# Kernel optimization log

Hardware: AMD Instinct MI355X
Metric: run time of the kernel (lower is better)

The kernel has to match this reference:

```python
import jax, jax.numpy as jnp
import numpy as np

HIDDEN = 2048
NH = 32        # query heads
NKV = 4        # kv heads
D = 128        # head dim
T = 2048       # tokens
WINDOW = 512   # sliding window
EPS = 1e-6
THETA = 1000000.0
SCALE = D ** -0.5


def setup_inputs() -> dict:
    key = jax.random.key(0)
    k1, k2, k3 = jax.random.split(key, 3)
    return {
        "positions": jnp.arange(T, dtype=jnp.int64) if jax.config.jax_enable_x64 else jnp.arange(T, dtype=jnp.int32),
        "hidden_states": jax.random.normal(k1, (T, HIDDEN), dtype=jnp.float32),
        "w_qkv": jax.random.normal(k2, (HIDDEN, (NH + 2 * NKV) * D), dtype=jnp.float32) * 0.02,
        "w_o": jax.random.normal(k3, (NH * D, HIDDEN), dtype=jnp.float32) * 0.02,
        "q_norm_w": jnp.ones((D,), dtype=jnp.float32),
        "k_norm_w": jnp.ones((D,), dtype=jnp.float32),
    }


def _rms_norm(x, w):
    # x: [..., D]; per-head RMSNorm
    var = jnp.mean(x * x, axis=-1, keepdims=True)
    return x * jax.lax.rsqrt(var + EPS) * w


def _rope(x, positions):
    # x: [T, H, D], neox-style rotary over full head dim
    inv_freq = 1.0 / (THETA ** (jnp.arange(0, D, 2, dtype=jnp.float32) / D))  # [D/2]
    freqs = positions.astype(jnp.float32)[:, None] * inv_freq                 # [T, D/2]
    cos = jnp.cos(freqs)[:, None, :]
    sin = jnp.sin(freqs)[:, None, :]
    x1, x2 = x[..., : D // 2], x[..., D // 2 :]
    return jnp.concatenate([x1 * cos - x2 * sin, x2 * cos + x1 * sin], axis=-1)


def reference(positions, hidden_states, w_qkv, w_o, q_norm_w, k_norm_w):
    qkv = hidden_states @ w_qkv                                   # [T, (NH+2NKV)*D]
    q, k, v = jnp.split(qkv, [NH * D, (NH + NKV) * D], axis=-1)
    q = _rms_norm(q.reshape(T, NH, D), q_norm_w)
    k = _rms_norm(k.reshape(T, NKV, D), k_norm_w)
    v = v.reshape(T, NKV, D)
    q = _rope(q, positions)
    k = _rope(k, positions)
    # GQA: expand kv heads to query heads
    rep = NH // NKV
    k = jnp.repeat(k, rep, axis=1)                                # [T, NH, D]
    v = jnp.repeat(v, rep, axis=1)
    scores = jnp.einsum("qhd,khd->hqk", q, k) * SCALE             # [NH, T, T]
    i = jnp.arange(T)[:, None]
    j = jnp.arange(T)[None, :]
    mask = (j <= i) & (i - j < WINDOW)                            # causal sliding window
    scores = jnp.where(mask[None, :, :], scores, jnp.finfo(scores.dtype).min)
    probs = jax.nn.softmax(scores, axis=-1)
    out = jnp.einsum("hqk,khd->qhd", probs, v).reshape(T, NH * D)
    return out @ w_o
```

## Files before the change

### kernel.cpp

```cpp
#include <hip/hip_runtime.h>
#include <math.h>

#define T      2048
#define HIDDEN 2048
#define NH     32
#define NKV    4
#define D      128
#define WINDOW 512
#define QKVW   ((NH + 2 * NKV) * D)
#define ODIM   (NH * D)
#define EPS    1e-6f
#define SCALE  0.08838834764831845f
#define PSTR   68
#define ESTR   136
#define QMUL   ((float)(0.08838834764831845 * 1.4426950408889634))
#define MLOG2E 5.7707801635558536f

typedef _Float16 f16x8 __attribute__((ext_vector_type(8)));
typedef float    f32x4 __attribute__((ext_vector_type(4)));


__global__ __launch_bounds__(256)
void pack_a(const float* __restrict__ A, _Float16* __restrict__ out,
            int M, int K) {
  const int cid = blockIdx.x * 256 + threadIdx.x;
  const int c = cid & 63;
  const int tile = cid >> 6;
  const int mtg = tile % (M >> 4);
  const int kt = tile / (M >> 4);
  const int m = c & 15, q = c >> 4;
  const float* src = A + (size_t)(mtg * 16 + m) * K + kt * 32 + q * 8;
  const float4 a = *(const float4*)src;
  const float4 b = *(const float4*)(src + 4);
  f16x8 h;
  h[0] = (_Float16)a.x; h[1] = (_Float16)a.y; h[2] = (_Float16)a.z; h[3] = (_Float16)a.w;
  h[4] = (_Float16)b.x; h[5] = (_Float16)b.y; h[6] = (_Float16)b.z; h[7] = (_Float16)b.w;
  *(f16x8*)(out + (size_t)cid * 8) = h;
}

__global__ __launch_bounds__(256)
void pack_b(const float* __restrict__ B, _Float16* __restrict__ out,
            int K, int N) {
  const int cid = blockIdx.x * 256 + threadIdx.x;
  const int c = cid & 63;
  const int tile = cid >> 6;
  const int ntg = tile % (N >> 4);
  const int kt = tile / (N >> 4);
  const int n = c & 15, q = c >> 4;
  const float* src = B + (size_t)(kt * 32 + q * 8) * N + ntg * 16 + n;
  f16x8 h;
#pragma unroll
  for (int j = 0; j < 8; ++j) h[j] = (_Float16)src[(size_t)j * N];
  *(f16x8*)(out + (size_t)cid * 8) = h;
}

__device__ __forceinline__ void gl2lds16(const void* g, void* l) {
  __builtin_amdgcn_global_load_lds((const __attribute__((address_space(1))) void*)g,
                                   (__attribute__((address_space(3))) void*)l,
                                   16, 0, 0);
}

__global__ __launch_bounds__(256)
void gemm_qkv(const _Float16* __restrict__ Apk, const _Float16* __restrict__ Bpk,
              const float* __restrict__ qnw, const float* __restrict__ knw,
              const float* __restrict__ cosT, const float* __restrict__ sinT,
              _Float16* __restrict__ Qpk, _Float16* __restrict__ Kpk,
              _Float16* __restrict__ Vpk) {
  constexpr int AT = 8, BT = 8, RT = 4, CT = 4;
  constexpr int NKT = HIDDEN / 32;
  __shared__ _Float16 SM[17920];
  _Float16* As = SM;
  _Float16* Bs = SM + 8192;

  const int tid = threadIdx.x;
  const int lane = tid & 63;
  const int wv = tid >> 6;
  const int wr = wv & 1, wc = wv >> 1;
  const int l15 = lane & 15;
  const int l4 = lane >> 4;
  const int bx = blockIdx.x, by = blockIdx.y;

  f32x4 acc[RT][CT];
#pragma unroll
  for (int i = 0; i < RT; ++i)
#pragma unroll
    for (int j = 0; j < CT; ++j) acc[i][j] = (f32x4)0.f;

  const size_t Astep = (size_t)(T >> 4) * 1024;
  const size_t Bstep = (size_t)(QKVW >> 4) * 1024;
  const char* Ag = (const char*)Apk + (size_t)(by * AT) * 1024 + lane * 16;
  const char* Bg = (const char*)Bpk + (size_t)(bx * BT) * 1024 + lane * 16;

  for (int kt2 = 0; kt2 < NKT; kt2 += 2) {
    const char* a0 = Ag + (size_t)kt2 * Astep;
    const char* b0 = Bg + (size_t)kt2 * Bstep;
#pragma unroll
    for (int t = wv; t < 2 * (AT + BT); t += 4) {
      const int half = t >= (AT + BT);
      const int tt = half ? t - (AT + BT) : t;
      if (tt < AT)
        gl2lds16(a0 + half * Astep + (size_t)tt * 1024,
                 (char*)As + (half * AT + tt) * 1024);
      else
        gl2lds16(b0 + half * Bstep + (size_t)(tt - AT) * 1024,
                 (char*)Bs + (half * BT + (tt - AT)) * 1024);
    }
    __syncthreads();
#pragma unroll
    for (int h2 = 0; h2 < 2; ++h2) {
      f16x8 af[RT], bf[CT];
#pragma unroll
      for (int i = 0; i < RT; ++i)
        af[i] = *(const f16x8*)((const char*)As + (h2 * AT + wr * RT + i) * 1024 + lane * 16);
#pragma unroll
      for (int j = 0; j < CT; ++j)
        bf[j] = *(const f16x8*)((const char*)Bs + (h2 * BT + wc * CT + j) * 1024 + lane * 16);
#pragma unroll
      for (int i = 0; i < RT; ++i)
#pragma unroll
        for (int j = 0; j < CT; ++j)
          acc[i][j] = __builtin_amdgcn_mfma_f32_16x16x32_f16(af[i], bf[j], acc[i][j], 0, 0, 0);
    }
    __syncthreads();
  }

  _Float16* ex = SM;
  float* sums = (float*)(SM + 17408);

  if (bx < NH + NKV) {
    const bool isq = bx < NH;
    const float* w = isq ? qnw : knw;
    const float omul = isq ? QMUL : 1.0f;

#pragma unroll
    for (int i = 0; i < RT; ++i)
#pragma unroll
      for (int r = 0; r < 4; ++r) {
        float s = acc[i][0][r] * acc[i][0][r] + acc[i][1][r] * acc[i][1][r]
                + acc[i][2][r] * acc[i][2][r] + acc[i][3][r] * acc[i][3][r];
        s += __shfl_xor(s, 1); s += __shfl_xor(s, 2);
        s += __shfl_xor(s, 4); s += __shfl_xor(s, 8);
        if (l15 == 0) sums[wc * 128 + wr * 64 + i * 16 + l4 * 4 + r] = s;
      }
    __syncthreads();

    float wcol[4];
#pragma unroll
    for (int j = 0; j < 4; ++j) wcol[j] = w[wc * 64 + j * 16 + l15];
#pragma unroll
    for (int i = 0; i < RT; ++i)
#pragma unroll
      for (int r = 0; r < 4; ++r) {
        const int row = wr * 64 + i * 16 + l4 * 4 + r;
        const float rn = 1.0f / sqrtf((sums[row] + sums[128 + row]) * (1.0f / D) + EPS);
#pragma unroll
        for (int j = 0; j < 4; ++j) {
          acc[i][j][r] *= rn * wcol[j];
          ex[row * ESTR + wc * 64 + j * 16 + l15] = (_Float16)acc[i][j][r];
        }
      }
    __syncthreads();

    const float sgn = (wc == 0) ? -1.f : 1.f;
    const int poff = wc ? 0 : 64;
#pragma unroll
    for (int i = 0; i < RT; ++i)
#pragma unroll
      for (int r = 0; r < 4; ++r) {
        const int row = wr * 64 + i * 16 + l4 * 4 + r;
        const int t = by * 128 + row;
#pragma unroll
        for (int j = 0; j < 4; ++j) {
          const int jc = j * 16 + l15;
          const float c = cosT[t * 64 + jc];
          const float s = sinT[t * 64 + jc];
          const float pr = (float)ex[row * ESTR + jc + poff];
          acc[i][j][r] = acc[i][j][r] * c + sgn * pr * s;
        }
      }
    __syncthreads();

#pragma unroll
    for (int i = 0; i < RT; ++i)
#pragma unroll
      for (int r = 0; r < 4; ++r) {
        const int row = wr * 64 + i * 16 + l4 * 4 + r;
#pragma unroll
        for (int j = 0; j < 4; ++j)
          ex[row * ESTR + wc * 64 + j * 16 + l15] = (_Float16)(acc[i][j][r] * omul);
      }
    __syncthreads();

    const int hl = isq ? bx : bx - NH;
    _Float16* dst0 = isq ? Qpk : Kpk;
#pragma unroll
    for (int u = 0; u < 2; ++u) {
      const int qtl = wv * 2 + u;
#pragma unroll
      for (int ds = 0; ds < 4; ++ds) {
        const f16x8 frag = *(const f16x8*)(ex + (qtl * 16 + l15) * ESTR + ds * 32 + l4 * 8);
        *(f16x8*)(dst0 + ((size_t)(hl * 128 + by * 8 + qtl) * 4 + ds) * 512 + lane * 8) = frag;
      }
    }
  } else {
    const int kvh = bx - NH - NKV;
#pragma unroll
    for (int i = 0; i < RT; ++i)
#pragma unroll
      for (int r = 0; r < 4; ++r) {
        const int row = wr * 64 + i * 16 + l4 * 4 + r;
#pragma unroll
        for (int j = 0; j < 4; ++j)
          ex[row * ESTR + wc * 64 + j * 16 + l15] = (_Float16)acc[i][j][r];
      }
    __syncthreads();
#pragma unroll
    for (int u = 0; u < 8; ++u) {
      const int idx = wv + 4 * u;
      const int dt = idx & 7, ks = (idx >> 3) & 1, ktl = idx >> 4;
      f16x8 h8;
#pragma unroll
      for (int jj = 0; jj < 8; ++jj)
        h8[jj] = ex[(ktl * 64 + ks * 32 + l4 * 8 + jj) * ESTR + dt * 16 + l15];
      *(f16x8*)(Vpk + (((size_t)(kvh * 32 + by * 2 + ktl) * 2 + ks) * 8 + dt) * 512 + lane * 8) = h8;
    }
  }
}

template<int BN>
__global__ __launch_bounds__(256)
void gemm_f16(const _Float16* __restrict__ Apk, const _Float16* __restrict__ Bpk,
              float* __restrict__ C0, float* __restrict__ C1,
              int M, int N, int nkt) {
  constexpr int BM = 128;
  constexpr int AT = BM / 16;
  constexpr int BT = BN / 16;
  constexpr int RT = 4;
  constexpr int CT = BN / 32;
  __shared__ _Float16 As[2 * AT * 512];
  __shared__ _Float16 Bs[2 * BT * 512];

  const int tid = threadIdx.x;
  const int lane = tid & 63;
  const int wv = tid >> 6;
  const int wr = wv & 1, wc = wv >> 1;
  const int kt0 = blockIdx.z * nkt;
  float* __restrict__ C = blockIdx.z ? C1 : C0;

  f32x4 acc[RT][CT];
#pragma unroll
  for (int i = 0; i < RT; ++i)
#pragma unroll
    for (int j = 0; j < CT; ++j) acc[i][j] = (f32x4)0.f;

  const size_t Astep = (size_t)(M >> 4) * 1024;
  const size_t Bstep = (size_t)(N >> 4) * 1024;
  const char* Ag = (const char*)Apk + (size_t)kt0 * Astep +
                   (size_t)(blockIdx.y * AT) * 1024 + lane * 16;
  const char* Bg = (const char*)Bpk + (size_t)kt0 * Bstep +
                   (size_t)(blockIdx.x * BT) * 1024 + lane * 16;

  for (int kt2 = 0; kt2 < nkt; kt2 += 2) {
    const char* a0 = Ag + (size_t)kt2 * Astep;
    const char* b0 = Bg + (size_t)kt2 * Bstep;
#pragma unroll
    for (int t = wv; t < 2 * (AT + BT); t += 4) {
      const int half = t >= (AT + BT);
      const int tt = half ? t - (AT + BT) : t;
      if (tt < AT)
        gl2lds16(a0 + half * Astep + (size_t)tt * 1024,
                 (char*)As + (half * AT + tt) * 1024);
      else
        gl2lds16(b0 + half * Bstep + (size_t)(tt - AT) * 1024,
                 (char*)Bs + (half * BT + (tt - AT)) * 1024);
    }
    __syncthreads();

#pragma unroll
    for (int h2 = 0; h2 < 2; ++h2) {
      f16x8 af[RT], bf[CT];
#pragma unroll
      for (int i = 0; i < RT; ++i)
        af[i] = *(const f16x8*)((const char*)As + (h2 * AT + wr * RT + i) * 1024 + lane * 16);
#pragma unroll
      for (int j = 0; j < CT; ++j)
        bf[j] = *(const f16x8*)((const char*)Bs + (h2 * BT + wc * CT + j) * 1024 + lane * 16);
#pragma unroll
      for (int i = 0; i < RT; ++i)
#pragma unroll
        for (int j = 0; j < CT; ++j)
          acc[i][j] = __builtin_amdgcn_mfma_f32_16x16x32_f16(af[i], bf[j], acc[i][j], 0, 0, 0);
    }
    __syncthreads();
  }

  const int row0 = blockIdx.y * BM + wr * 64 + ((lane >> 4) << 2);
  const int col0 = blockIdx.x * BN + wc * (CT * 16) + (lane & 15);
#pragma unroll
  for (int i = 0; i < RT; ++i)
#pragma unroll
    for (int j = 0; j < CT; ++j) {
#pragma unroll
      for (int r = 0; r < 4; ++r)
        C[(size_t)(row0 + i * 16 + r) * N + col0 + j * 16] = acc[i][j][r];
    }
}

__global__ __launch_bounds__(256)
void reduce_add(const float4* __restrict__ a, const float4* __restrict__ b,
                float4* __restrict__ o, int n4) {
  for (int i = blockIdx.x * 256 + threadIdx.x; i < n4; i += gridDim.x * 256) {
    const float4 x = a[i], y = b[i];
    o[i] = make_float4(x.x + y.x, x.y + y.y, x.z + y.z, x.w + y.w);
  }
}

__global__ __launch_bounds__(64)
void rope_tables(const int* __restrict__ positions,
                 float* __restrict__ cosT, float* __restrict__ sinT) {
  const int j = threadIdx.x;
  const int p0 = blockIdx.x * 64;
  const float invf = (float)pow(1.0e6, -(double)j / 64.0);
#pragma unroll 4
  for (int i = 0; i < 64; ++i) {
    const int t = p0 + i;
    const float ang = (float)positions[t] * invf;
    cosT[t * 64 + j] = cosf(ang);
    sinT[t * 64 + j] = sinf(ang);
  }
}

__global__ __launch_bounds__(256)
void attn_mfma(const _Float16* __restrict__ Qpk, const _Float16* __restrict__ Kpk,
               const _Float16* __restrict__ Vpk, _Float16* __restrict__ Ap2) {
  const int h = blockIdx.x;
  const int q0 = blockIdx.y * 128;
  const int kvh = h >> 3;
  const int tid = threadIdx.x;
  const int lane = tid & 63;
  const int wv = tid >> 6;
  const int l15 = lane & 15;
  const int l4 = lane >> 4;

  __shared__ _Float16 SM[8192 + 8192 + 4 * 32 * PSTR];
  _Float16* Ks = SM;
  _Float16* Vs = SM + 8192;
  _Float16* Pw = SM + 16384 + wv * 32 * PSTR;

  f16x8 qfA[4], qfB[4];
  {
    const _Float16* qa = Qpk + ((size_t)h * 128 + (q0 >> 4) + wv * 2) * 2048 + lane * 8;
#pragma unroll
    for (int ds = 0; ds < 4; ++ds) {
      qfA[ds] = *(const f16x8*)(qa + ds * 512);
      qfB[ds] = *(const f16x8*)(qa + 2048 + ds * 512);
    }
  }

  f16x8 ones;
#pragma unroll
  for (int j = 0; j < 8; ++j) ones[j] = (_Float16)1.0f;

  f32x4 OA[8], OB[8];
#pragma unroll
  for (int dt = 0; dt < 8; ++dt) { OA[dt] = (f32x4)0.f; OB[dt] = (f32x4)0.f; }
  f32x4 LA = (f32x4)0.f, LB = (f32x4)0.f;

  int kstart = q0 - (WINDOW - 1);
  if (kstart < 0) kstart = 0;
  kstart &= ~63;

  for (int kt = kstart; kt < q0 + 128; kt += 64) {
    __syncthreads();
    const _Float16* Kg = Kpk + ((size_t)kvh * 128 + (kt >> 4)) * 2048 + lane * 8;
    const _Float16* Vg = Vpk + ((size_t)kvh * 32 + (kt >> 6)) * 8192 + lane * 8;
#pragma unroll
    for (int t = wv; t < 16; t += 4) {
      gl2lds16(Kg + t * 512, (char*)Ks + t * 1024);
      gl2lds16(Vg + t * 512, (char*)Vs + t * 1024);
    }
    __syncthreads();

    f32x4 sA[4], sB[4];
#pragma unroll
    for (int nt = 0; nt < 4; ++nt) { sA[nt] = (f32x4)(-MLOG2E); sB[nt] = (f32x4)(-MLOG2E); }
#pragma unroll
    for (int ds = 0; ds < 4; ++ds) {
#pragma unroll
      for (int nt = 0; nt < 4; ++nt) {
        const f16x8 kf = *(const f16x8*)(Ks + (nt * 4 + ds) * 512 + lane * 8);
        sA[nt] = __builtin_amdgcn_mfma_f32_16x16x32_f16(qfA[ds], kf, sA[nt], 0, 0, 0);
        sB[nt] = __builtin_amdgcn_mfma_f32_16x16x32_f16(qfB[ds], kf, sB[nt], 0, 0, 0);
      }
    }

    const int qbA = q0 + wv * 32 + l4 * 4;
    const int kb = kt + l15;
#pragma unroll
    for (int nt = 0; nt < 4; ++nt) {
      const int kidx = kb + nt * 16;
#pragma unroll
      for (int r = 0; r < 4; ++r) {
        float pA = __builtin_amdgcn_exp2f(sA[nt][r]);
        float pB = __builtin_amdgcn_exp2f(sB[nt][r]);
        pA = ((unsigned)(qbA + r - kidx) < WINDOW) ? pA : 0.f;
        pB = ((unsigned)(qbA + 16 + r - kidx) < WINDOW) ? pB : 0.f;
        Pw[(l4 * 4 + r) * PSTR + nt * 16 + l15] = (_Float16)pA;
        Pw[(16 + l4 * 4 + r) * PSTR + nt * 16 + l15] = (_Float16)pB;
      }
    }

#pragma unroll
    for (int ks = 0; ks < 2; ++ks) {
      const f16x8 pfA = *(const f16x8*)(Pw + l15 * PSTR + ks * 32 + l4 * 8);
      const f16x8 pfB = *(const f16x8*)(Pw + (16 + l15) * PSTR + ks * 32 + l4 * 8);
      LA = __builtin_amdgcn_mfma_f32_16x16x32_f16(pfA, ones, LA, 0, 0, 0);
      LB = __builtin_amdgcn_mfma_f32_16x16x32_f16(pfB, ones, LB, 0, 0, 0);
#pragma unroll
      for (int dt = 0; dt < 8; ++dt) {
        const f16x8 vf = *(const f16x8*)(Vs + (ks * 8 + dt) * 512 + lane * 8);
        OA[dt] = __builtin_amdgcn_mfma_f32_16x16x32_f16(pfA, vf, OA[dt], 0, 0, 0);
        OB[dt] = __builtin_amdgcn_mfma_f32_16x16x32_f16(pfB, vf, OB[dt], 0, 0, 0);
      }
    }
  }

  __syncthreads();
  _Float16* Tw = SM + wv * 16 * ESTR;
#pragma unroll
  for (int half = 0; half < 2; ++half) {
    const f32x4* O = half ? OB : OA;
    const f32x4  L = half ? LB : LA;
    float inv[4];
#pragma unroll
    for (int r = 0; r < 4; ++r) inv[r] = 1.0f / L[r];
#pragma unroll
    for (int dt = 0; dt < 8; ++dt)
#pragma unroll
      for (int r = 0; r < 4; ++r)
        Tw[(l4 * 4 + r) * ESTR + dt * 16 + l15] = (_Float16)(O[dt][r] * inv[r]);
    const int qt = (q0 >> 4) + wv * 2 + half;
#pragma unroll
    for (int ds = 0; ds < 4; ++ds) {
      const f16x8 frag = *(const f16x8*)(Tw + l15 * ESTR + ds * 32 + l4 * 8);
      *(f16x8*)(Ap2 + ((size_t)(h * 4 + ds) * 128 + qt) * 512 + lane * 8) = frag;
    }
  }
}

extern "C" void kernel_launch(void* const* d_in, const int* in_sizes, int n_in,
                              void* d_out, int out_size, void* d_ws, size_t ws_size,
                              hipStream_t stream) {
  const int*   positions = (const int*)d_in[0];
  const float* hidden    = (const float*)d_in[1];
  const float* w_qkv     = (const float*)d_in[2];
  const float* w_o       = (const float*)d_in[3];
  const float* q_norm_w  = (const float*)d_in[4];
  const float* k_norm_w  = (const float*)d_in[5];
  float* out = (float*)d_out;

  char* ws = (char*)d_ws;
  _Float16* Kpk = (_Float16*)ws;
  _Float16* Vpk = Kpk + (size_t)T * NKV * D;
  ws += (size_t)T * QKVW * 4;
  _Float16* Ap2 = (_Float16*)ws;
  float* P0 = (float*)(ws + (size_t)T * ODIM * 2);
  ws += (size_t)T * ODIM * 4;
  float* cosT = (float*)ws;  ws += (size_t)T * 64 * 4;
  float* sinT = (float*)ws;  ws += (size_t)T * 64 * 4;
  _Float16* Bp1 = (_Float16*)ws; ws += (size_t)HIDDEN * QKVW * 2;
  _Float16* Bp2 = (_Float16*)ws; ws += (size_t)ODIM * HIDDEN * 2;
  _Float16* Ah1 = (_Float16*)ws; ws += (size_t)T * HIDDEN * 2;
  _Float16* Qpk = (_Float16*)ws;
  float* P1 = (float*)Qpk;
  ws += (size_t)T * ODIM * 2;

  pack_a<<<dim3((size_t)T * HIDDEN / 8 / 256), 256, 0, stream>>>(hidden, Ah1, T, HIDDEN);
  pack_b<<<dim3((size_t)HIDDEN * QKVW / 8 / 256), 256, 0, stream>>>(w_qkv, Bp1, HIDDEN, QKVW);
  pack_b<<<dim3((size_t)ODIM * HIDDEN / 8 / 256), 256, 0, stream>>>(w_o, Bp2, ODIM, HIDDEN);
  rope_tables<<<dim3(T / 64), 64, 0, stream>>>(positions, cosT, sinT);

  gemm_qkv<<<dim3(QKVW / 128, T / 128), 256, 0, stream>>>(
      Ah1, Bp1, q_norm_w, k_norm_w, cosT, sinT, Qpk, Kpk, Vpk);

  attn_mfma<<<dim3(NH, T / 128), 256, 0, stream>>>(Qpk, Kpk, Vpk, Ap2);

  gemm_f16<128><<<dim3(HIDDEN / 128, T / 128, 2), 256, 0, stream>>>(
      Ap2, Bp2, P0, P1, T, HIDDEN, ODIM / 32 / 2);
  reduce_add<<<dim3(512), 256, 0, stream>>>((const float4*)P0, (const float4*)P1,
                                            (float4*)out, T * HIDDEN / 4);
}
```

Before: 323.6 us.

## Fuse pack/rope prep kernels and restructure QKV GEMM epilogue per-wave

Merges the three packing kernels and the rope-table kernel into one launch that dispatches work by block range. This removes launch overhead and lets the small rope work overlap with the packing. The QKV GEMM changes its wave layout so each wave owns 32 full rows (2x8 tiles) instead of a 2x2 split. RMSNorm and RoPE can then run in registers with a shuffle reduction and no block-wide syncs, and the V transpose uses per-wave LDS. In exchange, every wave now reads all B fragments per k-step, which raises LDS read traffic.

```diff
diff --git a/kernel.cpp b/kernel.cpp
--- a/kernel.cpp
+++ b/kernel.cpp
@@ -13,51 +13,79 @@
 #define SCALE  0.08838834764831845f
 #define PSTR   68
 #define ESTR   136
+#define VSTR   36
 #define QMUL   ((float)(0.08838834764831845 * 1.4426950408889634))
 #define MLOG2E 5.7707801635558536f
 
 typedef _Float16 f16x8 __attribute__((ext_vector_type(8)));
+typedef _Float16 f16x4 __attribute__((ext_vector_type(4)));
 typedef float    f32x4 __attribute__((ext_vector_type(4)));
 
-
-__global__ __launch_bounds__(256)
-void pack_a(const float* __restrict__ A, _Float16* __restrict__ out,
-            int M, int K) {
-  const int cid = blockIdx.x * 256 + threadIdx.x;
-  const int c = cid & 63;
-  const int tile = cid >> 6;
-  const int mtg = tile % (M >> 4);
-  const int kt = tile / (M >> 4);
-  const int m = c & 15, q = c >> 4;
-  const float* src = A + (size_t)(mtg * 16 + m) * K + kt * 32 + q * 8;
-  const float4 a = *(const float4*)src;
-  const float4 b = *(const float4*)(src + 4);
-  f16x8 h;
-  h[0] = (_Float16)a.x; h[1] = (_Float16)a.y; h[2] = (_Float16)a.z; h[3] = (_Float16)a.w;
-  h[4] = (_Float16)b.x; h[5] = (_Float16)b.y; h[6] = (_Float16)b.z; h[7] = (_Float16)b.w;
-  *(f16x8*)(out + (size_t)cid * 8) = h;
-}
-
-__global__ __launch_bounds__(256)
-void pack_b(const float* __restrict__ B, _Float16* __restrict__ out,
-            int K, int N) {
-  const int cid = blockIdx.x * 256 + threadIdx.x;
-  const int c = cid & 63;
-  const int tile = cid >> 6;
-  const int ntg = tile % (N >> 4);
-  const int kt = tile / (N >> 4);
-  const int n = c & 15, q = c >> 4;
-  const float* src = B + (size_t)(kt * 32 + q * 8) * N + ntg * 16 + n;
-  f16x8 h;
-#pragma unroll
-  for (int j = 0; j < 8; ++j) h[j] = (_Float16)src[(size_t)j * N];
-  *(f16x8*)(out + (size_t)cid * 8) = h;
-}
 
 __device__ __forceinline__ void gl2lds16(const void* g, void* l) {
   __builtin_amdgcn_global_load_lds((const __attribute__((address_space(1))) void*)g,
                                    (__attribute__((address_space(3))) void*)l,
                                    16, 0, 0);
+}
+
+#define NB_A  2048
+#define NB_B1 5120
+#define NB_B2 4096
+__global__ __launch_bounds__(256)
+void prep(const float* __restrict__ hidden, const float* __restrict__ w_qkv,
+          const float* __restrict__ w_o, const int* __restrict__ positions,
+          _Float16* __restrict__ Ah1, _Float16* __restrict__ Bp1,
+          _Float16* __restrict__ Bp2, float* __restrict__ cosT,
+          float* __restrict__ sinT) {
+  const int bx = blockIdx.x;
+  const int tid = threadIdx.x;
+  if (bx < NB_A) {
+    const int cid = bx * 256 + tid;
+    const int c = cid & 63;
+    const int tile = cid >> 6;
+    const int mtg = tile & (T / 16 - 1);
+    const int kt = tile >> 7;
+    const float* src = hidden + (size_t)(mtg * 16 + (c & 15)) * HIDDEN + kt * 32 + (c >> 4) * 8;
+    const float4 a = *(const float4*)src;
+    const float4 b = *(const float4*)(src + 4);
+    f16x8 h;
+    h[0] = (_Float16)a.x; h[1] = (_Float16)a.y; h[2] = (_Float16)a.z; h[3] = (_Float16)a.w;
+    h[4] = (_Float16)b.x; h[5] = (_Float16)b.y; h[6] = (_Float16)b.z; h[7] = (_Float16)b.w;
+    *(f16x8*)(Ah1 + (size_t)cid * 8) = h;
+  } else if (bx < NB_A + NB_B1) {
+    const int cid = (bx - NB_A) * 256 + tid;
+    const int c = cid & 63;
+    const int tile = cid >> 6;
+    const int ntg = tile % (QKVW >> 4);
+    const int kt = tile / (QKVW >> 4);
+    const float* src = w_qkv + (size_t)(kt * 32 + (c >> 4) * 8) * QKVW + ntg * 16 + (c & 15);
+    f16x8 h;
+#pragma unroll
+    for (int j = 0; j < 8; ++j) h[j] = (_Float16)src[(size_t)j * QKVW];
+    *(f16x8*)(Bp1 + (size_t)cid * 8) = h;
+  } else if (bx < NB_A + NB_B1 + NB_B2) {
+    const int cid = (bx - NB_A - NB_B1) * 256 + tid;
+    const int c = cid & 63;
+    const int tile = cid >> 6;
+    const int ntg = tile & (HIDDEN / 16 - 1);
+    const int kt = tile >> 7;
+    const float* src = w_o + (size_t)(kt * 32 + (c >> 4) * 8) * HIDDEN + ntg * 16 + (c & 15);
+    f16x8 h;
+#pragma unroll
+    for (int j = 0; j < 8; ++j) h[j] = (_Float16)src[(size_t)j * HIDDEN];
+    *(f16x8*)(Bp2 + (size_t)cid * 8) = h;
+  } else {
+    const int p0 = (bx - NB_A - NB_B1 - NB_B2) * 64 + (tid >> 6) * 16;
+    const int j = tid & 63;
+    const float invf = (float)pow(1.0e6, -(double)j / 64.0);
+#pragma unroll 4
+    for (int i = 0; i < 16; ++i) {
+      const int t = p0 + i;
+      const float ang = (float)positions[t] * invf;
+      cosT[t * 64 + j] = cosf(ang);
+      sinT[t * 64 + j] = sinf(ang);
+    }
+  }
 }
 
 __global__ __launch_bounds__(256)
@@ -66,163 +94,127 @@
               const float* __restrict__ cosT, const float* __restrict__ sinT,
               _Float16* __restrict__ Qpk, _Float16* __restrict__ Kpk,
               _Float16* __restrict__ Vpk) {
-  constexpr int AT = 8, BT = 8, RT = 4, CT = 4;
   constexpr int NKT = HIDDEN / 32;
-  __shared__ _Float16 SM[17920];
+  __shared__ _Float16 SM[18432];
   _Float16* As = SM;
   _Float16* Bs = SM + 8192;
 
   const int tid = threadIdx.x;
   const int lane = tid & 63;
   const int wv = tid >> 6;
-  const int wr = wv & 1, wc = wv >> 1;
   const int l15 = lane & 15;
   const int l4 = lane >> 4;
   const int bx = blockIdx.x, by = blockIdx.y;
 
-  f32x4 acc[RT][CT];
-#pragma unroll
-  for (int i = 0; i < RT; ++i)
-#pragma unroll
-    for (int j = 0; j < CT; ++j) acc[i][j] = (f32x4)0.f;
+  f32x4 acc[2][8];
+#pragma unroll
+  for (int i = 0; i < 2; ++i)
+#pragma unroll
+    for (int j = 0; j < 8; ++j) acc[i][j] = (f32x4)0.f;
 
   const size_t Astep = (size_t)(T >> 4) * 1024;
   const size_t Bstep = (size_t)(QKVW >> 4) * 1024;
-  const char* Ag = (const char*)Apk + (size_t)(by * AT) * 1024 + lane * 16;
-  const char* Bg = (const char*)Bpk + (size_t)(bx * BT) * 1024 + lane * 16;
+  const char* Ag = (const char*)Apk + (size_t)(by * 8) * 1024 + lane * 16;
+  const char* Bg = (const char*)Bpk + (size_t)(bx * 8) * 1024 + lane * 16;
 
   for (int kt2 = 0; kt2 < NKT; kt2 += 2) {
     const char* a0 = Ag + (size_t)kt2 * Astep;
     const char* b0 = Bg + (size_t)kt2 * Bstep;
 #pragma unroll
-    for (int t = wv; t < 2 * (AT + BT); t += 4) {
-      const int half = t >= (AT + BT);
-      const int tt = half ? t - (AT + BT) : t;
-      if (tt < AT)
+    for (int t = wv; t < 32; t += 4) {
+      const int half = t >= 16;
+      const int tt = half ? t - 16 : t;
+      if (tt < 8)
         gl2lds16(a0 + half * Astep + (size_t)tt * 1024,
-                 (char*)As + (half * AT + tt) * 1024);
+                 (char*)As + (half * 8 + tt) * 1024);
       else
-        gl2lds16(b0 + half * Bstep + (size_t)(tt - AT) * 1024,
-                 (char*)Bs + (half * BT + (tt - AT)) * 1024);
+        gl2lds16(b0 + half * Bstep + (size_t)(tt - 8) * 1024,
+                 (char*)Bs + (half * 8 + (tt - 8)) * 1024);
     }
     __syncthreads();
 #pragma unroll
     for (int h2 = 0; h2 < 2; ++h2) {
-      f16x8 af[RT], bf[CT];
-#pragma unroll
-      for (int i = 0; i < RT; ++i)
-        af[i] = *(const f16x8*)((const char*)As + (h2 * AT + wr * RT + i) * 1024 + lane * 16);
-#pragma unroll
-      for (int j = 0; j < CT; ++j)
-        bf[j] = *(const f16x8*)((const char*)Bs + (h2 * BT + wc * CT + j) * 1024 + lane * 16);
-#pragma unroll
-      for (int i = 0; i < RT; ++i)
-#pragma unroll
-        for (int j = 0; j < CT; ++j)
+      f16x8 af[2], bf[8];
+#pragma unroll
+      for (int i = 0; i < 2; ++i)
+        af[i] = *(const f16x8*)(As + (h2 * 8 + wv * 2 + i) * 512 + lane * 8);
+#pragma unroll
+      for (int j = 0; j < 8; ++j)
+        bf[j] = *(const f16x8*)(Bs + (h2 * 8 + j) * 512 + lane * 8);
+#pragma unroll
+      for (int i = 0; i < 2; ++i)
+#pragma unroll
+        for (int j = 0; j < 8; ++j)
           acc[i][j] = __builtin_amdgcn_mfma_f32_16x16x32_f16(af[i], bf[j], acc[i][j], 0, 0, 0);
     }
     __syncthreads();
   }
-
-  _Float16* ex = SM;
-  float* sums = (float*)(SM + 17408);
 
   if (bx < NH + NKV) {
     const bool isq = bx < NH;
     const float* w = isq ? qnw : knw;
     const float omul = isq ? QMUL : 1.0f;
-
-#pragma unroll
-    for (int i = 0; i < RT; ++i)
+    float wcol[8];
+#pragma unroll
+    for (int j = 0; j < 8; ++j) wcol[j] = w[j * 16 + l15];
+
+    _Float16* ex = SM + wv * (32 * ESTR);
+#pragma unroll
+    for (int i = 0; i < 2; ++i)
 #pragma unroll
       for (int r = 0; r < 4; ++r) {
-        float s = acc[i][0][r] * acc[i][0][r] + acc[i][1][r] * acc[i][1][r]
-                + acc[i][2][r] * acc[i][2][r] + acc[i][3][r] * acc[i][3][r];
-        s += __shfl_xor(s, 1); s += __shfl_xor(s, 2);
-        s += __shfl_xor(s, 4); s += __shfl_xor(s, 8);
-        if (l15 == 0) sums[wc * 128 + wr * 64 + i * 16 + l4 * 4 + r] = s;
-      }
-    __syncthreads();
-
-    float wcol[4];
-#pragma unroll
-    for (int j = 0; j < 4; ++j) wcol[j] = w[wc * 64 + j * 16 + l15];
-#pragma unroll
-    for (int i = 0; i < RT; ++i)
-#pragma unroll
-      for (int r = 0; r < 4; ++r) {
-        const int row = wr * 64 + i * 16 + l4 * 4 + r;
-        const float rn = 1.0f / sqrtf((sums[row] + sums[128 + row]) * (1.0f / D) + EPS);
-#pragma unroll
-        for (int j = 0; j < 4; ++j) {
-          acc[i][j][r] *= rn * wcol[j];
-          ex[row * ESTR + wc * 64 + j * 16 + l15] = (_Float16)acc[i][j][r];
-        }
-      }
-    __syncthreads();
-
-    const float sgn = (wc == 0) ? -1.f : 1.f;
-    const int poff = wc ? 0 : 64;
-#pragma unroll
-    for (int i = 0; i < RT; ++i)
-#pragma unroll
-      for (int r = 0; r < 4; ++r) {
-        const int row = wr * 64 + i * 16 + l4 * 4 + r;
-        const int t = by * 128 + row;
+        float ss = 0.f;
+#pragma unroll
+        for (int j = 0; j < 8; ++j) ss += acc[i][j][r] * acc[i][j][r];
+        ss += __shfl_xor(ss, 1); ss += __shfl_xor(ss, 2);
+        ss += __shfl_xor(ss, 4); ss += __shfl_xor(ss, 8);
+        const float rn = 1.0f / sqrtf(ss * (1.0f / D) + EPS);
+        const int row = i * 16 + l4 * 4 + r;
+        const int t = by * 128 + wv * 32 + row;
 #pragma unroll
         for (int j = 0; j < 4; ++j) {
           const int jc = j * 16 + l15;
           const float c = cosT[t * 64 + jc];
           const float s = sinT[t * 64 + jc];
-          const float pr = (float)ex[row * ESTR + jc + poff];
-          acc[i][j][r] = acc[i][j][r] * c + sgn * pr * s;
+          const float x1 = acc[i][j][r] * rn * wcol[j];
+          const float x2 = acc[i][j + 4][r] * rn * wcol[j + 4];
+          ex[row * ESTR + jc]      = (_Float16)((x1 * c - x2 * s) * omul);
+          ex[row * ESTR + 64 + jc] = (_Float16)((x2 * c + x1 * s) * omul);
         }
       }
-    __syncthreads();
-
-#pragma unroll
-    for (int i = 0; i < RT; ++i)
-#pragma unroll
-      for (int r = 0; r < 4; ++r) {
-        const int row = wr * 64 + i * 16 + l4 * 4 + r;
-#pragma unroll
-        for (int j = 0; j < 4; ++j)
-          ex[row * ESTR + wc * 64 + j * 16 + l15] = (_Float16)(acc[i][j][r] * omul);
-      }
-    __syncthreads();
-
     const int hl = isq ? bx : bx - NH;
     _Float16* dst0 = isq ? Qpk : Kpk;
 #pragma unroll
     for (int u = 0; u < 2; ++u) {
-      const int qtl = wv * 2 + u;
+      const int qt = by * 8 + wv * 2 + u;
 #pragma unroll
       for (int ds = 0; ds < 4; ++ds) {
-        const f16x8 frag = *(const f16x8*)(ex + (qtl * 16 + l15) * ESTR + ds * 32 + l4 * 8);
-        *(f16x8*)(dst0 + ((size_t)(hl * 128 + by * 8 + qtl) * 4 + ds) * 512 + lane * 8) = frag;
+        const f16x8 frag = *(const f16x8*)(ex + (u * 16 + l15) * ESTR + ds * 32 + l4 * 8);
+        *(f16x8*)(dst0 + ((size_t)(hl * 128 + qt) * 4 + ds) * 512 + lane * 8) = frag;
       }
     }
   } else {
     const int kvh = bx - NH - NKV;
-#pragma unroll
-    for (int i = 0; i < RT; ++i)
-#pragma unroll
-      for (int r = 0; r < 4; ++r) {
-        const int row = wr * 64 + i * 16 + l4 * 4 + r;
-#pragma unroll
-        for (int j = 0; j < 4; ++j)
-          ex[row * ESTR + wc * 64 + j * 16 + l15] = (_Float16)acc[i][j][r];
-      }
-    __syncthreads();
-#pragma unroll
-    for (int u = 0; u < 8; ++u) {
-      const int idx = wv + 4 * u;
-      const int dt = idx & 7, ks = (idx >> 3) & 1, ktl = idx >> 4;
+    _Float16* exv = SM + wv * (128 * VSTR);
+#pragma unroll
+    for (int i = 0; i < 2; ++i)
+#pragma unroll
+      for (int j = 0; j < 8; ++j) {
+        f16x4 v4;
+#pragma unroll
+        for (int r = 0; r < 4; ++r) v4[r] = (_Float16)acc[i][j][r];
+        *(f16x4*)(exv + (j * 16 + l15) * VSTR + i * 16 + l4 * 4) = v4;
+      }
+    const int kt64 = by * 2 + (wv >> 1);
+    const int ks = wv & 1;
+#pragma unroll
+    for (int dt = 0; dt < 8; ++dt) {
+      const f16x4 lo = *(const f16x4*)(exv + (dt * 16 + l15) * VSTR + l4 * 8);
+      const f16x4 hi = *(const f16x4*)(exv + (dt * 16 + l15) * VSTR + l4 * 8 + 4);
       f16x8 h8;
 #pragma unroll
-      for (int jj = 0; jj < 8; ++jj)
-        h8[jj] = ex[(ktl * 64 + ks * 32 + l4 * 8 + jj) * ESTR + dt * 16 + l15];
-      *(f16x8*)(Vpk + (((size_t)(kvh * 32 + by * 2 + ktl) * 2 + ks) * 8 + dt) * 512 + lane * 8) = h8;
+      for (int r = 0; r < 4; ++r) { h8[r] = lo[r]; h8[r + 4] = hi[r]; }
+      *(f16x8*)(Vpk + (((size_t)(kvh * 32 + kt64) * 2 + ks) * 8 + dt) * 512 + lane * 8) = h8;
     }
   }
 }
@@ -312,21 +304,6 @@
   for (int i = blockIdx.x * 256 + threadIdx.x; i < n4; i += gridDim.x * 256) {
     const float4 x = a[i], y = b[i];
     o[i] = make_float4(x.x + y.x, x.y + y.y, x.z + y.z, x.w + y.w);
-  }
-}
-
-__global__ __launch_bounds__(64)
-void rope_tables(const int* __restrict__ positions,
-                 float* __restrict__ cosT, float* __restrict__ sinT) {
-  const int j = threadIdx.x;
-  const int p0 = blockIdx.x * 64;
-  const float invf = (float)pow(1.0e6, -(double)j / 64.0);
-#pragma unroll 4
-  for (int i = 0; i < 64; ++i) {
-    const int t = p0 + i;
-    const float ang = (float)positions[t] * invf;
-    cosT[t * 64 + j] = cosf(ang);
-    sinT[t * 64 + j] = sinf(ang);
   }
 }
 
@@ -475,10 +452,8 @@
   float* P1 = (float*)Qpk;
   ws += (size_t)T * ODIM * 2;
 
-  pack_a<<<dim3((size_t)T * HIDDEN / 8 / 256), 256, 0, stream>>>(hidden, Ah1, T, HIDDEN);
-  pack_b<<<dim3((size_t)HIDDEN * QKVW / 8 / 256), 256, 0, stream>>>(w_qkv, Bp1, HIDDEN, QKVW);
-  pack_b<<<dim3((size_t)ODIM * HIDDEN / 8 / 256), 256, 0, stream>>>(w_o, Bp2, ODIM, HIDDEN);
-  rope_tables<<<dim3(T / 64), 64, 0, stream>>>(positions, cosT, sinT);
+  prep<<<dim3(NB_A + NB_B1 + NB_B2 + T / 64), 256, 0, stream>>>(
+      hidden, w_qkv, w_o, positions, Ah1, Bp1, Bp2, cosT, sinT);
 
   gemm_qkv<<<dim3(QKVW / 128, T / 128), 256, 0, stream>>>(
       Ah1, Bp1, q_norm_w, k_norm_w, cosT, sinT, Qpk, Kpk, Vpk);
```

New measurement: 296.3 us. -8.4%, faster.
